# Kernel tuning notes

Hardware: AMD Instinct MI355X
Metric: run time of the kernel (lower is better)

## Reference

```python
import jax, jax.numpy as jnp
import numpy as np

NODES = 14      # input_size: nodes per graph
IN_F = 24       # seq_len: node feature dim
HID1 = 32
HID2 = 64       # hid_feats
HEADS = 2
OUT = 24        # output_size
B = 2048        # number of graphs
SLOPE = 0.2


def _make_edges():
    # fully connected (no self loops) within each 14-node graph
    pairs = np.array([(i, j) for i in range(NODES) for j in range(NODES) if i != j]).T  # [2,182]
    offs = (np.arange(B) * NODES)[:, None]
    src = (pairs[0][None, :] + offs).reshape(-1)
    dst = (pairs[1][None, :] + offs).reshape(-1)
    return np.stack([src, dst]).astype(np.int32)  # [2, 372736]


def setup_inputs() -> dict:
    key = jax.random.key(0)
    ks = jax.random.split(key, 16)
    N = B * NODES
    x = jax.random.normal(ks[0], (N, IN_F), dtype=jnp.float32)
    y = jax.random.normal(ks[1], (N, OUT), dtype=jnp.float32)
    edge_index = jnp.asarray(_make_edges())
    batch = jnp.repeat(jnp.arange(B, dtype=jnp.int32), NODES)
    s = 0.1
    params = dict(
        W1=jax.random.normal(ks[2], (IN_F, HEADS * HID1), dtype=jnp.float32) * s,
        a_src1=jax.random.normal(ks[3], (HEADS, HID1), dtype=jnp.float32) * s,
        a_dst1=jax.random.normal(ks[4], (HEADS, HID1), dtype=jnp.float32) * s,
        b1=jnp.zeros((HID1,), dtype=jnp.float32),
        W2=jax.random.normal(ks[5], (HID1, HEADS * HID2), dtype=jnp.float32) * s,
        a_src2=jax.random.normal(ks[6], (HEADS, HID2), dtype=jnp.float32) * s,
        a_dst2=jax.random.normal(ks[7], (HEADS, HID2), dtype=jnp.float32) * s,
        b2=jnp.zeros((HID2,), dtype=jnp.float32),
        Wf1=jax.random.normal(ks[8], (NODES, HID2, 8), dtype=jnp.float32) * s,
        bf1=jnp.zeros((NODES, 8), dtype=jnp.float32),
        Wf2=jax.random.normal(ks[9], (NODES, 8, OUT), dtype=jnp.float32) * s,
        bf2=jnp.zeros((NODES, OUT), dtype=jnp.float32),
    )
    return {"x": x, "y": y, "edge_index": edge_index, "batch": batch, **params}


def gat_conv(x, src, dst, W, a_src, a_dst, b):
    # PyG GATConv, concat=False (mean over heads), self-loops already in src/dst
    N = x.shape[0]
    H, F = a_src.shape
    xh = (x @ W).reshape(N, H, F)                       # [N,H,F]
    al_s = (xh * a_src).sum(-1)                         # [N,H]
    al_d = (xh * a_dst).sum(-1)                         # [N,H]
    alpha = jax.nn.leaky_relu(al_s[src] + al_d[dst], SLOPE)  # [E,H]
    amax = jax.ops.segment_max(alpha, dst, num_segments=N)
    ex = jnp.exp(alpha - amax[dst])
    den = jax.ops.segment_sum(ex, dst, num_segments=N)
    w = ex / den[dst]                                   # softmax per target node
    out = jax.ops.segment_sum(w[:, :, None] * xh[src], dst, num_segments=N)  # [N,H,F]
    return out.mean(axis=1) + b


def reference(x, y, edge_index, batch, W1, a_src1, a_dst1, b1, W2, a_src2, a_dst2, b2, Wf1, bf1, Wf2, bf2):
    N = x.shape[0]
    loops = jnp.arange(N, dtype=edge_index.dtype)
    src = jnp.concatenate([edge_index[0], loops])
    dst = jnp.concatenate([edge_index[1], loops])
    h = jax.nn.elu(gat_conv(x, src, dst, W1, a_src1, a_dst1, b1))   # [N,32]
    h = gat_conv(h, src, dst, W2, a_src2, a_dst2, b2)               # [N,64]
    # batch regroup: batch ids are contiguous per graph, so the Python
    # gather-loop in the original is exactly a reshape
    nb = N // NODES
    xg = h.reshape(nb, NODES, HID2).transpose(1, 0, 2)   # [14, B, 64]
    yg = y.reshape(nb, NODES, OUT)                       # [B, 14, out]
    # per-node-index MLP ensemble, batched over the 14 indices
    hh = jax.nn.relu(jnp.einsum('kbh,kho->kbo', xg, Wf1) + bf1[:, None, :])
    pred = jax.nn.sigmoid(jnp.einsum('kbo,kop->kbp', hh, Wf2) + bf2[:, None, :])  # [14,B,out]
    return pred, yg
```

## Files before the change

### kernel.cpp

```cpp
#include <hip/hip_runtime.h>

#define NODES 14
#define IN_F 24
#define HID1 32
#define HID2 64
#define OUT_F 24
#define SLOPE 0.2f

__global__ __launch_bounds__(64) void gnn_fused(
    const float* __restrict__ x, const float* __restrict__ y,
    const float* __restrict__ W1, const float* __restrict__ a_src1,
    const float* __restrict__ a_dst1, const float* __restrict__ b1,
    const float* __restrict__ W2, const float* __restrict__ a_src2,
    const float* __restrict__ a_dst2, const float* __restrict__ b2,
    const float* __restrict__ Wf1, const float* __restrict__ bf1,
    const float* __restrict__ Wf2, const float* __restrict__ bf2,
    float* __restrict__ out, int ngraphs)
{
  const int g = blockIdx.x;
  const int tid = threadIdx.x;

  __shared__ __align__(16) float xs[NODES * IN_F];
  __shared__ float als[NODES * 2];
  __shared__ float ald[NODES * 2];
  __shared__ float watt[NODES * NODES * 2];
  __shared__ __align__(16) float h1s[NODES * HID1];
  __shared__ __align__(16) float h2s[NODES * 68];
  __shared__ float hhs[NODES * 8];

  {
    const float4* y4 = (const float4*)(y + (size_t)g * (NODES * OUT_F));
    float4* o4 = (float4*)(out + (size_t)NODES * ngraphs * OUT_F
                               + (size_t)g * (NODES * OUT_F));
#pragma unroll
    for (int idx = tid; idx < (NODES * OUT_F) / 4; idx += 64)
      o4[idx] = y4[idx];
  }

  {
    const float4* x4 = (const float4*)(x + (size_t)g * (NODES * IN_F));
    float4* s4 = (float4*)xs;
#pragma unroll
    for (int idx = tid; idx < (NODES * IN_F) / 4; idx += 64)
      s4[idx] = x4[idx];
  }
  __syncthreads();

  float xcol[NODES];
  {
    float w[IN_F];
#pragma unroll
    for (int k = 0; k < IN_F; ++k) w[k] = W1[k * 64 + tid];
    const float asrc = a_src1[tid];
    const float adst = a_dst1[tid];
    const int h = tid >> 5, f5 = tid & 31;
#pragma unroll
    for (int n = 0; n < NODES; ++n) {
      float acc = 0.f;
#pragma unroll
      for (int k4 = 0; k4 < IN_F / 4; ++k4) {
        const float4 xv = *(const float4*)&xs[n * IN_F + k4 * 4];
        acc += xv.x * w[k4 * 4 + 0] + xv.y * w[k4 * 4 + 1]
             + xv.z * w[k4 * 4 + 2] + xv.w * w[k4 * 4 + 3];
      }
      xcol[n] = acc;
      float s = acc * asrc, d = acc * adst;
#pragma unroll
      for (int off = 1; off < 32; off <<= 1) {
        s += __shfl_xor(s, off);
        d += __shfl_xor(d, off);
      }
      if (f5 == 0) { als[n * 2 + h] = s; ald[n * 2 + h] = d; }
    }
  }
  __syncthreads();

  if (tid < NODES * 2) {
    const int j = tid >> 1, h = tid & 1;
    const float ad = ald[j * 2 + h];
    float a[NODES]; float m = -1e30f;
#pragma unroll
    for (int i = 0; i < NODES; ++i) {
      float v = als[i * 2 + h] + ad;
      v = v > 0.f ? v : SLOPE * v;
      a[i] = v; m = fmaxf(m, v);
    }
    float den = 0.f;
#pragma unroll
    for (int i = 0; i < NODES; ++i) { a[i] = __expf(a[i] - m); den += a[i]; }
    const float r = 1.f / den;
#pragma unroll
    for (int i = 0; i < NODES; ++i) watt[i * 28 + tid] = a[i] * r;
  }
  __syncthreads();

  {
    const int h = tid >> 5, f5 = tid & 31;
    const float bb = b1[f5];
#pragma unroll
    for (int n = 0; n < NODES; ++n) {
      float o = 0.f;
#pragma unroll
      for (int i = 0; i < NODES; ++i)
        o += watt[i * 28 + n * 2 + h] * xcol[i];
      const float other = __shfl_xor(o, 32);
      if (h == 0) {
        const float v = 0.5f * (o + other) + bb;
        h1s[n * HID1 + f5] = v > 0.f ? v : expm1f(v);
      }
    }
  }
  __syncthreads();

  float x2c0[NODES], x2c1[NODES];
  {
    float w2[HID1];
#pragma unroll
    for (int k = 0; k < HID1; ++k) w2[k] = W2[k * 128 + tid];
    {
      const float as2 = a_src2[tid], ad2 = a_dst2[tid];
#pragma unroll
      for (int n = 0; n < NODES; ++n) {
        float acc = 0.f;
#pragma unroll
        for (int k4 = 0; k4 < HID1 / 4; ++k4) {
          const float4 hv = *(const float4*)&h1s[n * HID1 + k4 * 4];
          acc += hv.x * w2[k4 * 4 + 0] + hv.y * w2[k4 * 4 + 1]
               + hv.z * w2[k4 * 4 + 2] + hv.w * w2[k4 * 4 + 3];
        }
        x2c0[n] = acc;
        float s = acc * as2, d = acc * ad2;
#pragma unroll
        for (int off = 1; off < 64; off <<= 1) {
          s += __shfl_xor(s, off);
          d += __shfl_xor(d, off);
        }
        if (tid == 0) { als[n * 2 + 0] = s; ald[n * 2 + 0] = d; }
      }
    }
#pragma unroll
    for (int k = 0; k < HID1; ++k) w2[k] = W2[k * 128 + 64 + tid];
    {
      const float as2 = a_src2[64 + tid], ad2 = a_dst2[64 + tid];
#pragma unroll
      for (int n = 0; n < NODES; ++n) {
        float acc = 0.f;
#pragma unroll
        for (int k4 = 0; k4 < HID1 / 4; ++k4) {
          const float4 hv = *(const float4*)&h1s[n * HID1 + k4 * 4];
          acc += hv.x * w2[k4 * 4 + 0] + hv.y * w2[k4 * 4 + 1]
               + hv.z * w2[k4 * 4 + 2] + hv.w * w2[k4 * 4 + 3];
        }
        x2c1[n] = acc;
        float s = acc * as2, d = acc * ad2;
#pragma unroll
        for (int off = 1; off < 64; off <<= 1) {
          s += __shfl_xor(s, off);
          d += __shfl_xor(d, off);
        }
        if (tid == 0) { als[n * 2 + 1] = s; ald[n * 2 + 1] = d; }
      }
    }
  }
  __syncthreads();

  if (tid < NODES * 2) {
    const int j = tid >> 1, h = tid & 1;
    const float ad = ald[j * 2 + h];
    float a[NODES]; float m = -1e30f;
#pragma unroll
    for (int i = 0; i < NODES; ++i) {
      float v = als[i * 2 + h] + ad;
      v = v > 0.f ? v : SLOPE * v;
      a[i] = v; m = fmaxf(m, v);
    }
    float den = 0.f;
#pragma unroll
    for (int i = 0; i < NODES; ++i) { a[i] = __expf(a[i] - m); den += a[i]; }
    const float r = 1.f / den;
#pragma unroll
    for (int i = 0; i < NODES; ++i) watt[i * 28 + tid] = a[i] * r;
  }
  __syncthreads();

  {
    const float bb = b2[tid];
#pragma unroll
    for (int n = 0; n < NODES; ++n) {
      float o0 = 0.f, o1 = 0.f;
#pragma unroll
      for (int i = 0; i < NODES; ++i) {
        const float2 wv = *(const float2*)&watt[i * 28 + n * 2];
        o0 += wv.x * x2c0[i];
        o1 += wv.y * x2c1[i];
      }
      h2s[n * 68 + tid] = 0.5f * (o0 + o1) + bb;
    }
  }
  __syncthreads();

  for (int idx = tid; idx < NODES * 8; idx += 64) {
    const int k = idx >> 3, e = idx & 7;
    float acc = bf1[k * 8 + e];
#pragma unroll
    for (int f = 0; f < HID2; ++f)
      acc += h2s[k * 68 + f] * Wf1[(k * HID2 + f) * 8 + e];
    hhs[idx] = fmaxf(acc, 0.f);
  }
  __syncthreads();

  for (int idx = tid; idx < NODES * OUT_F; idx += 64) {
    const int k = idx / OUT_F, o = idx % OUT_F;
    float acc = bf2[k * OUT_F + o];
#pragma unroll
    for (int e = 0; e < 8; ++e)
      acc += hhs[k * 8 + e] * Wf2[(k * 8 + e) * OUT_F + o];
    const float p = 1.f / (1.f + __expf(-acc));
    out[(size_t)k * ngraphs * OUT_F + (size_t)g * OUT_F + o] = p;
  }
}

extern "C" void kernel_launch(void* const* d_in, const int* in_sizes, int n_in,
                              void* d_out, int out_size, void* d_ws, size_t ws_size,
                              hipStream_t stream) {
  const float* x      = (const float*)d_in[0];
  const float* y      = (const float*)d_in[1];
  const float* W1     = (const float*)d_in[4];
  const float* a_src1 = (const float*)d_in[5];
  const float* a_dst1 = (const float*)d_in[6];
  const float* b1     = (const float*)d_in[7];
  const float* W2     = (const float*)d_in[8];
  const float* a_src2 = (const float*)d_in[9];
  const float* a_dst2 = (const float*)d_in[10];
  const float* b2     = (const float*)d_in[11];
  const float* Wf1    = (const float*)d_in[12];
  const float* bf1    = (const float*)d_in[13];
  const float* Wf2    = (const float*)d_in[14];
  const float* bf2    = (const float*)d_in[15];
  float* out = (float*)d_out;

  const int nnodes  = in_sizes[0] / IN_F;
  const int ngraphs = nnodes / NODES;

  hipLaunchKernelGGL(gnn_fused, dim3(ngraphs), dim3(64), 0, stream,
                     x, y, W1, a_src1, a_dst1, b1, W2, a_src2, a_dst2, b2,
                     Wf1, bf1, Wf2, bf2, out, ngraphs);
}
```

Measured before the change: 36.01 us.

## Fold attention vectors into weights and split heads across two wavefronts

Measured after the change: 63.33 us. 75.9% more time.

```diff
diff --git a/kernel.cpp b/kernel.cpp
--- a/kernel.cpp
+++ b/kernel.cpp
@@ -7,7 +7,11 @@
 #define OUT_F 24
 #define SLOPE 0.2f
 
-__global__ __launch_bounds__(64) void gnn_fused(
+#define XS_S 28
+#define H1_S 36
+#define H2_S 68
+
+__global__ __launch_bounds__(128) void gnn_fused(
     const float* __restrict__ x, const float* __restrict__ y,
     const float* __restrict__ W1, const float* __restrict__ a_src1,
     const float* __restrict__ a_dst1, const float* __restrict__ b1,
@@ -19,30 +23,51 @@
 {
   const int g = blockIdx.x;
   const int tid = threadIdx.x;
-
-  __shared__ __align__(16) float xs[NODES * IN_F];
-  __shared__ float als[NODES * 2];
-  __shared__ float ald[NODES * 2];
+  const int lane = tid & 63;
+  const int wid = tid >> 6;
+
+  __shared__ __align__(16) float xs[NODES * XS_S];
+  __shared__ float us1[2 * IN_F], ud1[2 * IN_F];
+  __shared__ float us2[2 * HID1], ud2[2 * HID1];
+  __shared__ float als[NODES * 2], ald[NODES * 2];
   __shared__ float watt[NODES * NODES * 2];
-  __shared__ __align__(16) float h1s[NODES * HID1];
-  __shared__ __align__(16) float h2s[NODES * 68];
+  __shared__ __align__(16) float h1s[NODES * H1_S];
+  __shared__ float h2s[NODES * H2_S];
   __shared__ float hhs[NODES * 8];
 
   {
     const float4* y4 = (const float4*)(y + (size_t)g * (NODES * OUT_F));
     float4* o4 = (float4*)(out + (size_t)NODES * ngraphs * OUT_F
                                + (size_t)g * (NODES * OUT_F));
-#pragma unroll
-    for (int idx = tid; idx < (NODES * OUT_F) / 4; idx += 64)
-      o4[idx] = y4[idx];
-  }
-
-  {
-    const float4* x4 = (const float4*)(x + (size_t)g * (NODES * IN_F));
-    float4* s4 = (float4*)xs;
-#pragma unroll
-    for (int idx = tid; idx < (NODES * IN_F) / 4; idx += 64)
-      s4[idx] = x4[idx];
+    if (tid < (NODES * OUT_F) / 4) o4[tid] = y4[tid];
+  }
+
+  for (int i = tid; i < NODES * IN_F; i += 128) {
+    const int n = i / IN_F, k = i - n * IN_F;
+    xs[n * XS_S + k] = x[(size_t)g * (NODES * IN_F) + i];
+  }
+
+  for (int it = tid; it < 224; it += 128) {
+    if (it < 96) {
+      const int sd = (it >= 48), r = it - sd * 48;
+      const int h = (r >= 24), k = r - h * 24;
+      const float* av = sd ? a_dst1 : a_src1;
+      float s = 0.f;
+#pragma unroll
+      for (int f = 0; f < HID1; ++f)
+        s += W1[k * 64 + h * HID1 + f] * av[h * HID1 + f];
+      (sd ? ud1 : us1)[h * IN_F + k] = s;
+    } else {
+      const int j = it - 96;
+      const int sd = (j >= 64), r = j - sd * 64;
+      const int h = (r >= 32), k = r - h * 32;
+      const float* av = sd ? a_dst2 : a_src2;
+      float s = 0.f;
+#pragma unroll
+      for (int f = 0; f < HID2; ++f)
+        s += W2[k * 128 + h * HID2 + f] * av[h * HID2 + f];
+      (sd ? ud2 : us2)[h * HID1 + k] = s;
+    }
   }
   __syncthreads();
 
@@ -50,28 +75,27 @@
   {
     float w[IN_F];
 #pragma unroll
-    for (int k = 0; k < IN_F; ++k) w[k] = W1[k * 64 + tid];
-    const float asrc = a_src1[tid];
-    const float adst = a_dst1[tid];
-    const int h = tid >> 5, f5 = tid & 31;
+    for (int k = 0; k < IN_F; ++k) w[k] = W1[k * 64 + lane];
 #pragma unroll
     for (int n = 0; n < NODES; ++n) {
       float acc = 0.f;
 #pragma unroll
       for (int k4 = 0; k4 < IN_F / 4; ++k4) {
-        const float4 xv = *(const float4*)&xs[n * IN_F + k4 * 4];
+        const float4 xv = *(const float4*)&xs[n * XS_S + k4 * 4];
         acc += xv.x * w[k4 * 4 + 0] + xv.y * w[k4 * 4 + 1]
              + xv.z * w[k4 * 4 + 2] + xv.w * w[k4 * 4 + 3];
       }
       xcol[n] = acc;
-      float s = acc * asrc, d = acc * adst;
-#pragma unroll
-      for (int off = 1; off < 32; off <<= 1) {
-        s += __shfl_xor(s, off);
-        d += __shfl_xor(d, off);
-      }
-      if (f5 == 0) { als[n * 2 + h] = s; ald[n * 2 + h] = d; }
-    }
+    }
+  }
+
+  if (tid < 56) {
+    const int n = tid >> 2, h = (tid >> 1) & 1, sd = tid & 1;
+    const float* uu = sd ? ud1 : us1;
+    float s = 0.f;
+#pragma unroll
+    for (int k = 0; k < IN_F; ++k) s += xs[n * XS_S + k] * uu[h * IN_F + k];
+    (sd ? ald : als)[n * 2 + h] = s;
   }
   __syncthreads();
 
@@ -95,72 +119,49 @@
   __syncthreads();
 
   {
-    const int h = tid >> 5, f5 = tid & 31;
+    const int h = lane >> 5, f5 = lane & 31;
     const float bb = b1[f5];
 #pragma unroll
-    for (int n = 0; n < NODES; ++n) {
+    for (int t = 0; t < NODES / 2; ++t) {
+      const int n = wid * (NODES / 2) + t;
       float o = 0.f;
 #pragma unroll
       for (int i = 0; i < NODES; ++i)
         o += watt[i * 28 + n * 2 + h] * xcol[i];
-      const float other = __shfl_xor(o, 32);
+      const float oo = __shfl_xor(o, 32);
       if (h == 0) {
-        const float v = 0.5f * (o + other) + bb;
-        h1s[n * HID1 + f5] = v > 0.f ? v : expm1f(v);
+        const float v = 0.5f * (o + oo) + bb;
+        h1s[n * H1_S + f5] = v > 0.f ? v : expm1f(v);
       }
     }
   }
   __syncthreads();
 
-  float x2c0[NODES], x2c1[NODES];
+  float x2c[NODES];
   {
     float w2[HID1];
 #pragma unroll
     for (int k = 0; k < HID1; ++k) w2[k] = W2[k * 128 + tid];
-    {
-      const float as2 = a_src2[tid], ad2 = a_dst2[tid];
-#pragma unroll
-      for (int n = 0; n < NODES; ++n) {
-        float acc = 0.f;
-#pragma unroll
-        for (int k4 = 0; k4 < HID1 / 4; ++k4) {
-          const float4 hv = *(const float4*)&h1s[n * HID1 + k4 * 4];
-          acc += hv.x * w2[k4 * 4 + 0] + hv.y * w2[k4 * 4 + 1]
-               + hv.z * w2[k4 * 4 + 2] + hv.w * w2[k4 * 4 + 3];
-        }
-        x2c0[n] = acc;
-        float s = acc * as2, d = acc * ad2;
-#pragma unroll
-        for (int off = 1; off < 64; off <<= 1) {
-          s += __shfl_xor(s, off);
-          d += __shfl_xor(d, off);
-        }
-        if (tid == 0) { als[n * 2 + 0] = s; ald[n * 2 + 0] = d; }
+#pragma unroll
+    for (int n = 0; n < NODES; ++n) {
+      float acc = 0.f;
+#pragma unroll
+      for (int k4 = 0; k4 < HID1 / 4; ++k4) {
+        const float4 hv = *(const float4*)&h1s[n * H1_S + k4 * 4];
+        acc += hv.x * w2[k4 * 4 + 0] + hv.y * w2[k4 * 4 + 1]
+             + hv.z * w2[k4 * 4 + 2] + hv.w * w2[k4 * 4 + 3];
       }
-    }
-#pragma unroll
-    for (int k = 0; k < HID1; ++k) w2[k] = W2[k * 128 + 64 + tid];
-    {
-      const float as2 = a_src2[64 + tid], ad2 = a_dst2[64 + tid];
-#pragma unroll
-      for (int n = 0; n < NODES; ++n) {
-        float acc = 0.f;
-#pragma unroll
-        for (int k4 = 0; k4 < HID1 / 4; ++k4) {
-          const float4 hv = *(const float4*)&h1s[n * HID1 + k4 * 4];
-          acc += hv.x * w2[k4 * 4 + 0] + hv.y * w2[k4 * 4 + 1]
-               + hv.z * w2[k4 * 4 + 2] + hv.w * w2[k4 * 4 + 3];
-        }
-        x2c1[n] = acc;
-        float s = acc * as2, d = acc * ad2;
-#pragma unroll
-        for (int off = 1; off < 64; off <<= 1) {
-          s += __shfl_xor(s, off);
-          d += __shfl_xor(d, off);
-        }
-        if (tid == 0) { als[n * 2 + 1] = s; ald[n * 2 + 1] = d; }
-      }
-    }
+      x2c[n] = acc;
+    }
+  }
+
+  if (tid < 56) {
+    const int n = tid >> 2, h = (tid >> 1) & 1, sd = tid & 1;
+    const float* uu = sd ? ud2 : us2;
+    float s = 0.f;
+#pragma unroll
+    for (int k = 0; k < HID1; ++k) s += h1s[n * H1_S + k] * uu[h * HID1 + k];
+    (sd ? ald : als)[n * 2 + h] = s;
   }
   __syncthreads();
 
@@ -184,39 +185,47 @@
   __syncthreads();
 
   {
-    const float bb = b2[tid];
+    float agg[NODES];
 #pragma unroll
     for (int n = 0; n < NODES; ++n) {
-      float o0 = 0.f, o1 = 0.f;
-#pragma unroll
-      for (int i = 0; i < NODES; ++i) {
-        const float2 wv = *(const float2*)&watt[i * 28 + n * 2];
-        o0 += wv.x * x2c0[i];
-        o1 += wv.y * x2c1[i];
-      }
-      h2s[n * 68 + tid] = 0.5f * (o0 + o1) + bb;
-    }
-  }
-  __syncthreads();
-
-  for (int idx = tid; idx < NODES * 8; idx += 64) {
-    const int k = idx >> 3, e = idx & 7;
+      float o = 0.f;
+#pragma unroll
+      for (int i = 0; i < NODES; ++i)
+        o += watt[i * 28 + n * 2 + wid] * x2c[i];
+      agg[n] = o;
+    }
+    if (wid == 1) {
+#pragma unroll
+      for (int n = 0; n < NODES; ++n) h2s[n * H2_S + lane] = agg[n];
+    }
+    __syncthreads();
+    if (wid == 0) {
+      const float bb = b2[lane];
+#pragma unroll
+      for (int n = 0; n < NODES; ++n)
+        h2s[n * H2_S + lane] = 0.5f * (agg[n] + h2s[n * H2_S + lane]) + bb;
+    }
+  }
+  __syncthreads();
+
+  if (tid < NODES * 8) {
+    const int k = tid >> 3, e = tid & 7;
     float acc = bf1[k * 8 + e];
 #pragma unroll
     for (int f = 0; f < HID2; ++f)
-      acc += h2s[k * 68 + f] * Wf1[(k * HID2 + f) * 8 + e];
-    hhs[idx] = fmaxf(acc, 0.f);
-  }
-  __syncthreads();
-
-  for (int idx = tid; idx < NODES * OUT_F; idx += 64) {
-    const int k = idx / OUT_F, o = idx % OUT_F;
+      acc += h2s[k * H2_S + f] * Wf1[(k * HID2 + f) * 8 + e];
+    hhs[tid] = fmaxf(acc, 0.f);
+  }
+  __syncthreads();
+
+  for (int idx = tid; idx < NODES * OUT_F; idx += 128) {
+    const int k = idx / OUT_F, o = idx - k * OUT_F;
     float acc = bf2[k * OUT_F + o];
 #pragma unroll
     for (int e = 0; e < 8; ++e)
       acc += hhs[k * 8 + e] * Wf2[(k * 8 + e) * OUT_F + o];
-    const float p = 1.f / (1.f + __expf(-acc));
-    out[(size_t)k * ngraphs * OUT_F + (size_t)g * OUT_F + o] = p;
+    out[(size_t)k * ngraphs * OUT_F + (size_t)g * OUT_F + o] =
+        1.f / (1.f + __expf(-acc));
   }
 }
 
@@ -242,7 +251,7 @@
   const int nnodes  = in_sizes[0] / IN_F;
   const int ngraphs = nnodes / NODES;
 
-  hipLaunchKernelGGL(gnn_fused, dim3(ngraphs), dim3(64), 0, stream,
+  hipLaunchKernelGGL(gnn_fused, dim3(ngraphs), dim3(128), 0, stream,
                      x, y, W1, a_src1, a_dst1, b1, W2, a_src2, a_dst2, b2,
                      Wf1, bf1, Wf2, bf2, out, ngraphs);
 }
```
